# Kernel optimization log

Measured on AMD Instinct MI355X. Metric: run time of the kernel, lower is better.

Reference implementation:

```python
import jax, jax.numpy as jnp
import numpy as np

N_HEADS = 4
NUM_GROUPS = 32
EPS = 1e-6


def _nin(t, W, b):
    # 1x1 conv as dense over channel dim: [B,C,H,W] x [C,D] -> [B,D,H,W]
    return jnp.einsum('bchw,cd->bdhw', t, W) + b[None, :, None, None]


def setup_inputs() -> dict:
    key = jax.random.key(0)
    ks = jax.random.split(key, 12)
    B, C, H, W = 8, 256, 32, 32
    Tc = 512
    Cin = C + Tc  # 768
    x = jax.random.normal(ks[0], (B, C, H, W), dtype=jnp.float32)
    text_feat = jax.random.normal(ks[1], (B, Tc), dtype=jnp.float32)
    gn_gamma = jnp.ones((Cin,), dtype=jnp.float32)
    gn_beta = jnp.zeros((Cin,), dtype=jnp.float32)
    scale = 1.0 / np.sqrt(Cin)
    W0 = jax.random.normal(ks[2], (Cin, C), dtype=jnp.float32) * scale
    b0 = jnp.zeros((C,), dtype=jnp.float32)
    W1 = jax.random.normal(ks[3], (Cin, C), dtype=jnp.float32) * scale
    b1 = jnp.zeros((C,), dtype=jnp.float32)
    W2 = jax.random.normal(ks[4], (Cin, C), dtype=jnp.float32) * scale
    b2 = jnp.zeros((C,), dtype=jnp.float32)
    return {"x": x, "text_feat": text_feat, "gn_gamma": gn_gamma, "gn_beta": gn_beta,
            "W0": W0, "b0": b0, "W1": W1, "b1": b1, "W2": W2, "b2": b2}


def reference(x, text_feat, gn_gamma, gn_beta, W0, b0, W1, b1, W2, b2):
    B, C, H, W = x.shape
    # broadcast text features spatially and concat on channel dim
    tf = jnp.broadcast_to(text_feat[:, :, None, None], (B, text_feat.shape[1], H, W))
    h = jnp.concatenate([x, tf], axis=1)  # [B, C+Tc, H, W]
    Ctot = h.shape[1]
    # GroupNorm(32, Ctot), eps=1e-6
    hg = h.reshape(B, NUM_GROUPS, Ctot // NUM_GROUPS, H, W)
    mu = hg.mean(axis=(2, 3, 4), keepdims=True)
    var = hg.var(axis=(2, 3, 4), keepdims=True)
    hn = ((hg - mu) * jax.lax.rsqrt(var + EPS)).reshape(B, Ctot, H, W)
    hn = hn * gn_gamma[None, :, None, None] + gn_beta[None, :, None, None]
    q = _nin(hn, W0, b0)
    k = _nin(hn, W1, b1)
    v = _nin(hn, W2, b2)
    Ch = C // N_HEADS
    qh = q.reshape(B * N_HEADS, Ch, H, W)
    kh = k.reshape(B * N_HEADS, Ch, H, W)
    vh = v.reshape(B * N_HEADS, Ch, H, W)
    # full HW x HW attention scores, softmax over flattened key positions
    w = jnp.einsum('bchw,bcij->bhwij', qh, kh) * (Ch ** -0.5)
    w = jax.nn.softmax(w.reshape(B * N_HEADS, H, W, H * W), axis=-1)
    w = w.reshape(B * N_HEADS, H, W, H, W)
    ho = jnp.einsum('bhwij,bcij->bchw', w, vh).reshape(B, C, H, W)
    return x + ho
```

## Files before the change

kernel.cpp:

```cpp
#include <hip/hip_runtime.h>
#include <math.h>

#define BATCH 8
#define CX 256
#define TC 512
#define CIN 768
#define HW_TOT 1024
#define NH 4
#define CHD 64

typedef __attribute__((ext_vector_type(8))) short short8;
typedef __attribute__((ext_vector_type(4))) short s4v;
typedef __attribute__((ext_vector_type(4))) float floatx4;
typedef __attribute__((ext_vector_type(4))) int int4v;

#define QSCALE 0.18033688f

static __device__ __forceinline__ short f2bf(float f) {
    union { float f; unsigned u; } c; c.f = f;
    unsigned r = (c.u + 0x7fffu + ((c.u >> 16) & 1u)) >> 16;
    return (short)r;
}

static __device__ __forceinline__ int pack_trunc(float lo, float hi) {
    union { float f; unsigned u; } L, H;
    L.f = lo; H.f = hi;
    return (int)((H.u & 0xffff0000u) | (L.u >> 16));
}

__global__ __launch_bounds__(256)
void gn_kernel(const float* __restrict__ x, const float* __restrict__ tf,
               const float* __restrict__ gamma, const float* __restrict__ beta,
               float* __restrict__ scale, float* __restrict__ shift,
               float* __restrict__ tc) {
    const int b = blockIdx.x >> 5;
    const int g = blockIdx.x & 31;
    const int t = threadIdx.x;
    const int w = t >> 6, lane = t & 63;
    if (blockIdx.x < 24) tc[blockIdx.x * 256 + t] = 0.f;

    float s = 0.f, ss = 0.f;
    #pragma unroll
    for (int rr = 0; rr < 6; rr++) {
        const int row = w * 6 + rr;
        const int cg = g * 24 + row;
        if (cg < CX) {
            const float4* p = (const float4*)(x + ((size_t)b * CX + cg) * HW_TOT);
            #pragma unroll
            for (int i = 0; i < 4; i++) {
                float4 v = p[lane + 64 * i];
                s += v.x + v.y + v.z + v.w;
                ss += v.x * v.x + v.y * v.y + v.z * v.z + v.w * v.w;
            }
        } else {
            float v = tf[b * TC + cg - CX];
            s += 16.f * v;
            ss += 16.f * v * v;
        }
    }
    #pragma unroll
    for (int d = 1; d < 64; d <<= 1) {
        s += __shfl_xor(s, d);
        ss += __shfl_xor(ss, d);
    }
    __shared__ float rs_[4], rss_[4];
    if (lane == 0) { rs_[w] = s; rss_[w] = ss; }
    __syncthreads();
    const float S  = rs_[0] + rs_[1] + rs_[2] + rs_[3];
    const float SS = rss_[0] + rss_[1] + rss_[2] + rss_[3];
    const float inv_n = 1.f / (24 * 1024);
    const float mean = S * inv_n;
    const float var = SS * inv_n - mean * mean;
    const float r = rsqrtf(var + 1e-6f);
    if (t < 24) {
        int cg = g * 24 + t;
        float sc = gamma[cg] * r;
        scale[b * CIN + cg] = sc;
        shift[b * CIN + cg] = beta[cg] - mean * sc;
    }
}

__global__ __launch_bounds__(256)
void prep_kernel(const float* __restrict__ x, const float* __restrict__ tf,
                 const float* __restrict__ scale, const float* __restrict__ shift,
                 const float* __restrict__ W0, const float* __restrict__ W1,
                 const float* __restrict__ W2,
                 short* __restrict__ hnT, short* __restrict__ Wt,
                 float* __restrict__ tc) {
    __shared__ float hs[128];
    __shared__ float red[4][64];
    const int bx = blockIdx.x;
    const int t = threadIdx.x;
    if (bx < 256) {
        int id = (bx & 31) * 256 + t;
        int b = id >> 10;
        const float* xb = x + (size_t)b * CX * HW_TOT + (id & 1023);
        const float* scb = scale + b * CIN;
        const float* shb = shift + b * CIN;
        short* outp = hnT + (size_t)id * CX;
        int c0base = (bx >> 5) * 32;
        for (int c0 = c0base; c0 < c0base + 32; c0 += 8) {
            short8 o;
            #pragma unroll
            for (int i = 0; i < 8; i++) {
                float v = xb[(size_t)(c0 + i) * HW_TOT];
                o[i] = f2bf(v * scb[c0 + i] + shb[c0 + i]);
            }
            *(short8*)(outp + c0) = o;
        }
    } else if (bx < 268) {
        int m = bx - 256;
        int dg = (m % 3) * 256 + t;
        int which = dg >> 8, d = dg & 255;
        const float* Wm = (which == 0) ? W0 : (which == 1) ? W1 : W2;
        int c0base = (m / 3) * 64;
        for (int c0 = c0base; c0 < c0base + 64; c0 += 8) {
            short8 o;
            #pragma unroll
            for (int i = 0; i < 8; i++) o[i] = f2bf(Wm[(size_t)(c0 + i) * CX + d]);
            *(short8*)(Wt + (size_t)dg * CX + c0) = o;
        }
    } else {
        int m = bx - 268;
        int ks = m & 3;
        int b = (m >> 2) & 7, dt = m >> 5;
        int which = dt >> 2, d0 = (dt & 3) * 64;
        const float* Wm = (which == 0) ? W0 : (which == 1) ? W1 : W2;
        if (t < 128) {
            int c = ks * 128 + t;
            hs[t] = tf[b * TC + c] * scale[b * CIN + CX + c] + shift[b * CIN + CX + c];
        }
        __syncthreads();
        int td = t & 63, tq = t >> 6;
        float acc = 0.f;
        const float* wp = Wm + (size_t)(CX + ks * 128 + tq * 32) * CX + d0 + td;
        #pragma unroll 8
        for (int c = 0; c < 32; c++)
            acc = fmaf(hs[tq * 32 + c], wp[(size_t)c * CX], acc);
        red[tq][td] = acc;
        __syncthreads();
        if (t < 64)
            atomicAdd(&tc[b * CIN + which * CX + d0 + t],
                      red[0][t] + red[1][t] + red[2][t] + red[3][t]);
    }
}

__global__ __launch_bounds__(256)
void qkv_gemm(const short* __restrict__ hnT, const short* __restrict__ Wt,
              const float* __restrict__ tc,
              const float* __restrict__ b0, const float* __restrict__ b1,
              const float* __restrict__ b2,
              short* __restrict__ qb, short* __restrict__ kb, short* __restrict__ vb) {
    const int hw0 = blockIdx.x * 64, dt = blockIdx.y, b = blockIdx.z;
    const int which = dt >> 2;
    const int col0 = (dt & 3) * 64;
    const int dg0 = which * 256 + col0;
    const bool OV = (which == 2);

    __shared__ short At[64 * 72];
    __shared__ short Bt[64 * 72];

    const int t = threadIdx.x;
    const int w = t >> 6, l = t & 63;
    const int wm = w >> 1, wn = w & 1;
    const int l15 = l & 15, q = l >> 4;
    const int srow = t >> 2, sch = (t & 3) * 16;

    const short* gA = hnT + (size_t)(b * HW_TOT + hw0 + srow) * CX + sch;
    const short* gB = Wt + (size_t)(dg0 + srow) * CX + sch;

    floatx4 acc[2][2] = {};
    for (int k0 = 0; k0 < CX; k0 += 64) {
        __syncthreads();
        *(short8*)(At + srow * 72 + sch)     = *(const short8*)(gA + k0);
        *(short8*)(At + srow * 72 + sch + 8) = *(const short8*)(gA + k0 + 8);
        *(short8*)(Bt + srow * 72 + sch)     = *(const short8*)(gB + k0);
        *(short8*)(Bt + srow * 72 + sch + 8) = *(const short8*)(gB + k0 + 8);
        __syncthreads();
        const short* aB = OV ? Bt : At;
        const short* bB = OV ? At : Bt;
        #pragma unroll
        for (int kc = 0; kc < 2; kc++) {
            short8 af[2], bf2[2];
            #pragma unroll
            for (int mt = 0; mt < 2; mt++)
                af[mt] = *(const short8*)(aB + (wm * 32 + mt * 16 + l15) * 72 + kc * 32 + q * 8);
            #pragma unroll
            for (int nt = 0; nt < 2; nt++)
                bf2[nt] = *(const short8*)(bB + (wn * 32 + nt * 16 + l15) * 72 + kc * 32 + q * 8);
            #pragma unroll
            for (int mt = 0; mt < 2; mt++)
                #pragma unroll
                for (int nt = 0; nt < 2; nt++)
                    acc[mt][nt] = __builtin_amdgcn_mfma_f32_16x16x32_bf16(
                        af[mt], bf2[nt], acc[mt][nt], 0, 0, 0);
        }
    }

    __syncthreads();
    const float* bias = (which == 0) ? b0 : (which == 1) ? b1 : b2;
    if (!OV) {
        const float qs = (which == 0) ? QSCALE : 1.0f;
        float cadd[2];
        #pragma unroll
        for (int nt = 0; nt < 2; nt++) {
            int d = col0 + wn * 32 + nt * 16 + l15;
            cadd[nt] = bias[d] + tc[b * CIN + which * CX + d];
        }
        #pragma unroll
        for (int mt = 0; mt < 2; mt++)
            #pragma unroll
            for (int rr = 0; rr < 4; rr++)
                #pragma unroll
                for (int nt = 0; nt < 2; nt++)
                    At[(wm * 32 + mt * 16 + q * 4 + rr) * 72 + wn * 32 + nt * 16 + l15]
                        = f2bf((acc[mt][nt][rr] + cadd[nt]) * qs);
    } else {
        #pragma unroll
        for (int mt = 0; mt < 2; mt++)
            #pragma unroll
            for (int rr = 0; rr < 4; rr++) {
                int d = col0 + wm * 32 + mt * 16 + q * 4 + rr;
                float radd = bias[d] + tc[b * CIN + 2 * CX + d];
                #pragma unroll
                for (int nt = 0; nt < 2; nt++)
                    At[(wm * 32 + mt * 16 + q * 4 + rr) * 72 + wn * 32 + nt * 16 + l15]
                        = f2bf(acc[mt][nt][rr] + radd);
            }
    }
    __syncthreads();
    short8 v0 = *(const short8*)(At + srow * 72 + sch);
    short8 v1 = *(const short8*)(At + srow * 72 + sch + 8);
    if (!OV) {
        short* outp = (which == 0) ? qb : kb;
        size_t off = (size_t)(b * HW_TOT + hw0 + srow) * CX + col0 + sch;
        *(short8*)(outp + off) = v0;
        *(short8*)(outp + off + 8) = v1;
    } else {
        size_t off = (size_t)(b * CX + col0 + srow) * HW_TOT + hw0 + sch;
        *(short8*)(vb + off) = v0;
        *(short8*)(vb + off + 8) = v1;
    }
}

__global__ __launch_bounds__(256, 3)
void attn_kernel(const short* __restrict__ qb, const short* __restrict__ kb,
                 const short* __restrict__ vb, const float* __restrict__ x,
                 float* __restrict__ out) {
    const int qt = blockIdx.x, bh = blockIdx.y;
    const int b = bh >> 2, h = bh & 3;
    const int hw0 = qt * 64;

    __shared__ short Qs[64 * 72];
    __shared__ short Ks[2][64 * 72];
    __shared__ short Vs[2][64 * 72];

    const int t = threadIdx.x;
    const int w = t >> 6, l = t & 63;
    const int pair = w >> 1, jh = w & 1;
    const int l15 = l & 15, q = l >> 4;
    const int srow = t >> 2, sch = (t & 3) * 16;
    const int vpos0 = ((sch >> 5) << 5) + ((sch >> 4) & 1) * 4;

    {
        const short* gq = qb + (size_t)(b * HW_TOT + hw0 + srow) * CX + h * CHD + sch;
        *(short8*)(Qs + srow * 72 + sch)     = *(const short8*)gq;
        *(short8*)(Qs + srow * 72 + sch + 8) = *(const short8*)(gq + 8);
    }

    short8 pk[2][2], pv[2][2];
    #pragma unroll
    for (int s = 0; s < 2; s++) {
        const int j0 = s * 512;
        const short* gk = kb + (size_t)(b * HW_TOT + j0 + srow) * CX + h * CHD + sch;
        pk[s][0] = *(const short8*)gk;
        pk[s][1] = *(const short8*)(gk + 8);
        const short* gv = vb + (size_t)(b * CX + h * CHD + srow) * HW_TOT + j0 + sch;
        pv[s][0] = *(const short8*)gv;
        pv[s][1] = *(const short8*)(gv + 8);
    }
    #pragma unroll
    for (int s = 0; s < 2; s++) {
        *(short8*)(Ks[s] + srow * 72 + sch)     = pk[s][0];
        *(short8*)(Ks[s] + srow * 72 + sch + 8) = pk[s][1];
        short* vrow = Vs[s] + srow * 72 + vpos0;
        *(s4v*)(vrow)      = __builtin_shufflevector(pv[s][0], pv[s][0], 0, 1, 2, 3);
        *(s4v*)(vrow + 8)  = __builtin_shufflevector(pv[s][0], pv[s][0], 4, 5, 6, 7);
        *(s4v*)(vrow + 16) = __builtin_shufflevector(pv[s][1], pv[s][1], 0, 1, 2, 3);
        *(s4v*)(vrow + 24) = __builtin_shufflevector(pv[s][1], pv[s][1], 4, 5, 6, 7);
    }
    __syncthreads();

    short8 aq[2][2];
    #pragma unroll
    for (int g = 0; g < 2; g++) {
        aq[g][0] = *(const short8*)(Qs + (pair * 32 + g * 16 + l15) * 72 + q * 8);
        aq[g][1] = *(const short8*)(Qs + (pair * 32 + g * 16 + l15) * 72 + 32 + q * 8);
    }

    union { int4v i; short8 s; } ones;
    ones.i[0] = 0x3f803f80; ones.i[1] = 0x3f803f80;
    ones.i[2] = 0x3f803f80; ones.i[3] = 0x3f803f80;

    floatx4 oacc[2][4] = {};
    floatx4 lacc[2] = {};
    const short* Kc = Ks[jh];
    const short* Vc = Vs[jh];

    for (int jj = 0; jj < 8; jj++) {
        if (jj < 7) {
            #pragma unroll
            for (int s = 0; s < 2; s++) {
                const int j0 = s * 512 + (jj + 1) * 64;
                const short* gk = kb + (size_t)(b * HW_TOT + j0 + srow) * CX + h * CHD + sch;
                pk[s][0] = *(const short8*)gk;
                pk[s][1] = *(const short8*)(gk + 8);
                const short* gv = vb + (size_t)(b * CX + h * CHD + srow) * HW_TOT + j0 + sch;
                pv[s][0] = *(const short8*)gv;
                pv[s][1] = *(const short8*)(gv + 8);
            }
        }

        floatx4 sacc[2][4] = {};
        #pragma unroll
        for (int nt = 0; nt < 4; nt++) {
            short8 kf0 = *(const short8*)(Kc + (nt * 16 + l15) * 72 + q * 8);
            short8 kf1 = *(const short8*)(Kc + (nt * 16 + l15) * 72 + 32 + q * 8);
            #pragma unroll
            for (int g = 0; g < 2; g++) {
                sacc[g][nt] = __builtin_amdgcn_mfma_f32_16x16x32_bf16(kf0, aq[g][0], sacc[g][nt], 0, 0, 0);
                sacc[g][nt] = __builtin_amdgcn_mfma_f32_16x16x32_bf16(kf1, aq[g][1], sacc[g][nt], 0, 0, 0);
            }
        }

        union { int4v i; short8 s; } u[2][2];
        #pragma unroll
        for (int g = 0; g < 2; g++)
            #pragma unroll
            for (int nt = 0; nt < 4; nt++) {
                float e0 = exp2f(sacc[g][nt][0]);
                float e1 = exp2f(sacc[g][nt][1]);
                float e2 = exp2f(sacc[g][nt][2]);
                float e3 = exp2f(sacc[g][nt][3]);
                u[g][nt >> 1].i[(nt & 1) * 2]     = pack_trunc(e0, e1);
                u[g][nt >> 1].i[(nt & 1) * 2 + 1] = pack_trunc(e2, e3);
            }

        #pragma unroll
        for (int g = 0; g < 2; g++) {
            lacc[g] = __builtin_amdgcn_mfma_f32_16x16x32_bf16(ones.s, u[g][0].s, lacc[g], 0, 0, 0);
            lacc[g] = __builtin_amdgcn_mfma_f32_16x16x32_bf16(ones.s, u[g][1].s, lacc[g], 0, 0, 0);
        }

        #pragma unroll
        for (int ct = 0; ct < 4; ct++) {
            const short* vr = Vc + (ct * 16 + l15) * 72;
            #pragma unroll
            for (int kcc = 0; kcc < 2; kcc++) {
                short8 vf = *(const short8*)(vr + kcc * 32 + q * 8);
                #pragma unroll
                for (int g = 0; g < 2; g++)
                    oacc[g][ct] = __builtin_amdgcn_mfma_f32_16x16x32_bf16(
                        vf, u[g][kcc].s, oacc[g][ct], 0, 0, 0);
            }
        }

        if (jj < 7) {
            __syncthreads();
            #pragma unroll
            for (int s = 0; s < 2; s++) {
                *(short8*)(Ks[s] + srow * 72 + sch)     = pk[s][0];
                *(short8*)(Ks[s] + srow * 72 + sch + 8) = pk[s][1];
                short* vrow = Vs[s] + srow * 72 + vpos0;
                *(s4v*)(vrow)      = __builtin_shufflevector(pv[s][0], pv[s][0], 0, 1, 2, 3);
                *(s4v*)(vrow + 8)  = __builtin_shufflevector(pv[s][0], pv[s][0], 4, 5, 6, 7);
                *(s4v*)(vrow + 16) = __builtin_shufflevector(pv[s][1], pv[s][1], 0, 1, 2, 3);
                *(s4v*)(vrow + 24) = __builtin_shufflevector(pv[s][1], pv[s][1], 4, 5, 6, 7);
            }
            __syncthreads();
        }
    }

    __syncthreads();
    float* Of = (float*)Ks;
    float* Lf = (float*)Vs;
    if (jh == 1) {
        #pragma unroll
        for (int g = 0; g < 2; g++) {
            int qi = pair * 32 + g * 16 + l15;
            #pragma unroll
            for (int ct = 0; ct < 4; ct++)
                *(floatx4*)&Of[qi * 68 + ct * 16 + q * 4] = oacc[g][ct];
            if (q == 0) Lf[qi] = lacc[g][0];
        }
    }
    __syncthreads();
    if (jh == 0) {
        #pragma unroll
        for (int g = 0; g < 2; g++) {
            int qi = pair * 32 + g * 16 + l15;
            const float rinv = 1.f / (lacc[g][0] + Lf[qi]);
            #pragma unroll
            for (int ct = 0; ct < 4; ct++) {
                floatx4 po = *(const floatx4*)&Of[qi * 68 + ct * 16 + q * 4];
                #pragma unroll
                for (int r = 0; r < 4; r++) {
                    int c = h * CHD + ct * 16 + q * 4 + r;
                    size_t idx = (size_t)(b * CX + c) * HW_TOT + hw0 + qi;
                    out[idx] = x[idx] + (oacc[g][ct][r] + po[r]) * rinv;
                }
            }
        }
    }
}

extern "C" void kernel_launch(void* const* d_in, const int* in_sizes, int n_in,
                              void* d_out, int out_size, void* d_ws, size_t ws_size,
                              hipStream_t stream) {
    (void)in_sizes; (void)n_in; (void)out_size; (void)ws_size;
    const float* x     = (const float*)d_in[0];
    const float* tf    = (const float*)d_in[1];
    const float* gamma = (const float*)d_in[2];
    const float* beta  = (const float*)d_in[3];
    const float* W0 = (const float*)d_in[4];
    const float* b0 = (const float*)d_in[5];
    const float* W1 = (const float*)d_in[6];
    const float* b1 = (const float*)d_in[7];
    const float* W2 = (const float*)d_in[8];
    const float* b2 = (const float*)d_in[9];

    char* ws = (char*)d_ws;
    float* scale  = (float*)(ws);
    float* shift  = (float*)(ws + 24576);
    float* tcb    = (float*)(ws + 49152);
    short* Wt     = (short*)(ws + 73728);
    short* hnT    = (short*)(ws + 466944);
    short* qb     = (short*)(ws + 4661248);
    short* kb     = (short*)(ws + 8855552);
    short* vb     = (short*)(ws + 13049856);

    hipLaunchKernelGGL(gn_kernel, dim3(256), dim3(256), 0, stream,
                       x, tf, gamma, beta, scale, shift, tcb);
    hipLaunchKernelGGL(prep_kernel, dim3(652), dim3(256), 0, stream,
                       x, tf, scale, shift, W0, W1, W2, hnT, Wt, tcb);
    hipLaunchKernelGGL(qkv_gemm, dim3(16, 12, BATCH), dim3(256), 0, stream,
                       hnT, Wt, tcb, b0, b1, b2, qb, kb, vb);
    hipLaunchKernelGGL(attn_kernel, dim3(16, 32), dim3(256), 0, stream,
                       qb, kb, vb, x, (float*)d_out);
}
```

Before: 118.3 us.

## Load full K panel into swizzled LDS in QKV GEMM; raise MFMA priority

The QKV GEMM now loads the entire 256-wide K dimension of both operand tiles into shared memory in one pass. It uses an XOR-swizzled layout in place of padding, which removes the per-iteration barriers of the 64-wide K loop. Occupancy is hinted at 2 blocks per CU and shared usage grows to 64 KB per block, so residency may drop. s_setprio hints are also wrapped around the MFMA sections in both the GEMM and attention kernels to favour matrix issue over other waves.

```diff
diff --git a/kernel.cpp b/kernel.cpp
--- a/kernel.cpp
+++ b/kernel.cpp
@@ -145,7 +145,7 @@
     }
 }
 
-__global__ __launch_bounds__(256)
+__global__ __launch_bounds__(256, 2)
 void qkv_gemm(const short* __restrict__ hnT, const short* __restrict__ Wt,
               const float* __restrict__ tc,
               const float* __restrict__ b0, const float* __restrict__ b1,
@@ -157,45 +157,59 @@
     const int dg0 = which * 256 + col0;
     const bool OV = (which == 2);
 
-    __shared__ short At[64 * 72];
-    __shared__ short Bt[64 * 72];
+    __shared__ short At[64 * 256];
+    __shared__ short Bt[64 * 256];
 
     const int t = threadIdx.x;
     const int w = t >> 6, l = t & 63;
     const int wm = w >> 1, wn = w & 1;
     const int l15 = l & 15, q = l >> 4;
-    const int srow = t >> 2, sch = (t & 3) * 16;
-
-    const short* gA = hnT + (size_t)(b * HW_TOT + hw0 + srow) * CX + sch;
-    const short* gB = Wt + (size_t)(dg0 + srow) * CX + sch;
+    const int srow = t >> 2;
+    const int cbase = (t & 3) * 8;
+    const int sw = srow & 7;
+
+    const short* gA = hnT + (size_t)(b * HW_TOT + hw0 + srow) * CX + cbase * 8;
+    const short* gB = Wt + (size_t)(dg0 + srow) * CX + cbase * 8;
+
+    short8 ra[8], rb[8];
+    #pragma unroll
+    for (int i = 0; i < 8; i++) ra[i] = *(const short8*)(gA + i * 8);
+    #pragma unroll
+    for (int i = 0; i < 8; i++) rb[i] = *(const short8*)(gB + i * 8);
+    short* wA = At + srow * 256;
+    short* wB = Bt + srow * 256;
+    #pragma unroll
+    for (int i = 0; i < 8; i++) *(short8*)(wA + ((cbase + i) ^ sw) * 8) = ra[i];
+    #pragma unroll
+    for (int i = 0; i < 8; i++) *(short8*)(wB + ((cbase + i) ^ sw) * 8) = rb[i];
+    __syncthreads();
+
+    const short* aB = OV ? Bt : At;
+    const short* bB = OV ? At : Bt;
 
     floatx4 acc[2][2] = {};
-    for (int k0 = 0; k0 < CX; k0 += 64) {
-        __syncthreads();
-        *(short8*)(At + srow * 72 + sch)     = *(const short8*)(gA + k0);
-        *(short8*)(At + srow * 72 + sch + 8) = *(const short8*)(gA + k0 + 8);
-        *(short8*)(Bt + srow * 72 + sch)     = *(const short8*)(gB + k0);
-        *(short8*)(Bt + srow * 72 + sch + 8) = *(const short8*)(gB + k0 + 8);
-        __syncthreads();
-        const short* aB = OV ? Bt : At;
-        const short* bB = OV ? At : Bt;
-        #pragma unroll
-        for (int kc = 0; kc < 2; kc++) {
-            short8 af[2], bf2[2];
-            #pragma unroll
-            for (int mt = 0; mt < 2; mt++)
-                af[mt] = *(const short8*)(aB + (wm * 32 + mt * 16 + l15) * 72 + kc * 32 + q * 8);
+    __builtin_amdgcn_s_setprio(1);
+    #pragma unroll
+    for (int kc = 0; kc < 8; kc++) {
+        short8 af[2], bf2[2];
+        #pragma unroll
+        for (int mt = 0; mt < 2; mt++) {
+            const int r = wm * 32 + mt * 16 + l15;
+            af[mt] = *(const short8*)(aB + r * 256 + ((kc * 4 + q) ^ (r & 7)) * 8);
+        }
+        #pragma unroll
+        for (int nt = 0; nt < 2; nt++) {
+            const int r = wn * 32 + nt * 16 + l15;
+            bf2[nt] = *(const short8*)(bB + r * 256 + ((kc * 4 + q) ^ (r & 7)) * 8);
+        }
+        #pragma unroll
+        for (int mt = 0; mt < 2; mt++)
             #pragma unroll
             for (int nt = 0; nt < 2; nt++)
-                bf2[nt] = *(const short8*)(bB + (wn * 32 + nt * 16 + l15) * 72 + kc * 32 + q * 8);
-            #pragma unroll
-            for (int mt = 0; mt < 2; mt++)
-                #pragma unroll
-                for (int nt = 0; nt < 2; nt++)
-                    acc[mt][nt] = __builtin_amdgcn_mfma_f32_16x16x32_bf16(
-                        af[mt], bf2[nt], acc[mt][nt], 0, 0, 0);
-        }
-    }
+                acc[mt][nt] = __builtin_amdgcn_mfma_f32_16x16x32_bf16(
+                    af[mt], bf2[nt], acc[mt][nt], 0, 0, 0);
+    }
+    __builtin_amdgcn_s_setprio(0);
 
     __syncthreads();
     const float* bias = (which == 0) ? b0 : (which == 1) ? b1 : b2;
@@ -229,15 +243,16 @@
             }
     }
     __syncthreads();
-    short8 v0 = *(const short8*)(At + srow * 72 + sch);
-    short8 v1 = *(const short8*)(At + srow * 72 + sch + 8);
+    const int sch2 = (t & 3) * 16;
+    short8 v0 = *(const short8*)(At + srow * 72 + sch2);
+    short8 v1 = *(const short8*)(At + srow * 72 + sch2 + 8);
     if (!OV) {
         short* outp = (which == 0) ? qb : kb;
-        size_t off = (size_t)(b * HW_TOT + hw0 + srow) * CX + col0 + sch;
+        size_t off = (size_t)(b * HW_TOT + hw0 + srow) * CX + col0 + sch2;
         *(short8*)(outp + off) = v0;
         *(short8*)(outp + off + 8) = v1;
     } else {
-        size_t off = (size_t)(b * CX + col0 + srow) * HW_TOT + hw0 + sch;
+        size_t off = (size_t)(b * CX + col0 + srow) * HW_TOT + hw0 + sch2;
         *(short8*)(vb + off) = v0;
         *(short8*)(vb + off + 8) = v1;
     }
@@ -322,6 +337,7 @@
         }
 
         floatx4 sacc[2][4] = {};
+        __builtin_amdgcn_s_setprio(1);
         #pragma unroll
         for (int nt = 0; nt < 4; nt++) {
             short8 kf0 = *(const short8*)(Kc + (nt * 16 + l15) * 72 + q * 8);
@@ -332,6 +348,7 @@
                 sacc[g][nt] = __builtin_amdgcn_mfma_f32_16x16x32_bf16(kf1, aq[g][1], sacc[g][nt], 0, 0, 0);
             }
         }
+        __builtin_amdgcn_s_setprio(0);
 
         union { int4v i; short8 s; } u[2][2];
         #pragma unroll
@@ -346,6 +363,7 @@
                 u[g][nt >> 1].i[(nt & 1) * 2 + 1] = pack_trunc(e2, e3);
             }
 
+        __builtin_amdgcn_s_setprio(1);
         #pragma unroll
         for (int g = 0; g < 2; g++) {
             lacc[g] = __builtin_amdgcn_mfma_f32_16x16x32_bf16(ones.s, u[g][0].s, lacc[g], 0, 0, 0);
@@ -364,6 +382,7 @@
                         vf, u[g][kcc].s, oacc[g][ct], 0, 0, 0);
             }
         }
+        __builtin_amdgcn_s_setprio(0);
 
         if (jj < 7) {
             __syncthreads();
```

Result: slower. 123.1 us (+4.0%).
